# Performance work log

Measured on AMD Instinct MI355X. Metric: run time of the kernel, lower is better.

## Reference

```python
import jax, jax.numpy as jnp
import numpy as np

N = 32768       # nodes
IN = 256        # in_channels
D = 128         # out_channels (per-head dim)
H = 4           # num_heads
M = 4           # num_reps (seeds per partition)
KP = 128        # number of partitions
S = N // KP     # partition size (equal-size partitions)
SCALE = float(np.sqrt(D))


def _linear_init(key, fan_in, fan_out):
    # torch nn.Linear default: U(-1/sqrt(fan_in), 1/sqrt(fan_in)) for W and b
    kw, kb = jax.random.split(key)
    bound = 1.0 / np.sqrt(fan_in)
    w = jax.random.uniform(kw, (fan_in, fan_out), jnp.float32, -bound, bound)
    b = jax.random.uniform(kb, (fan_out,), jnp.float32, -bound, bound)
    return w, b


def setup_inputs() -> dict:
    key = jax.random.key(0)
    k0, k1, k2, k3, k4 = jax.random.split(key, 5)
    x = jax.random.normal(k0, (N, IN), jnp.float32)
    # equal-size disjoint partitions: [KP, S] index array covering 0..N-1
    partition_indices = jnp.arange(N, dtype=jnp.int32).reshape(KP, S)
    Wq_w, Wq_b = _linear_init(k1, IN, H * D)
    Wk_w, Wk_b = _linear_init(k2, IN, H * D)
    Wv_w, Wv_b = _linear_init(k3, IN, H * D)
    pool_seeds = jax.random.normal(k4, (M, H, D), jnp.float32) * 0.02
    alpha_logit = jnp.float32(0.0)
    beta = jnp.float32(1.0)
    return {
        "x": x, "partition_indices": partition_indices,
        "Wq_w": Wq_w, "Wq_b": Wq_b, "Wk_w": Wk_w, "Wk_b": Wk_b,
        "Wv_w": Wv_w, "Wv_b": Wv_b, "pool_seeds": pool_seeds,
        "alpha_logit": alpha_logit, "beta": beta,
    }


def reference(x, partition_indices, Wq_w, Wq_b, Wk_w, Wk_b, Wv_w, Wv_b,
              pool_seeds, alpha_logit, beta):
    n = x.shape[0]
    Q = (x @ Wq_w + Wq_b).reshape(n, H, D)
    K = (x @ Wk_w + Wk_b).reshape(n, H, D)
    V = (x @ Wv_w + Wv_b).reshape(n, H, D)

    # gather per partition -> [KP, S, H, D]
    Qp = Q[partition_indices]
    Kp = K[partition_indices]
    Vp = V[partition_indices]

    # Fine: exact softmax attention within each partition
    attn_local = jnp.einsum('kphd,kqhd->khpq', Qp, Kp) / SCALE
    attn_local = jax.nn.softmax(attn_local, axis=-1)
    outp = jnp.einsum('khpq,kqhd->kphd', attn_local, Vp)  # [KP,S,H,D]
    # partitions are disjoint -> scatter-set back to node order
    out_local = jnp.zeros((n, H, D), x.dtype).at[partition_indices.reshape(-1)].set(
        outp.reshape(n, H, D))
    x_local = out_local.mean(axis=1)  # [N, D]

    # Coarse: learned seeds pool each partition
    pool_attn = jnp.einsum('mhd,kqhd->kmhq', pool_seeds, Kp) / SCALE
    pool_attn = jax.nn.softmax(pool_attn, axis=-1)
    reps_k = jnp.einsum('kmhq,kqhd->kmhd', pool_attn, Kp).reshape(KP * M, H, D)
    reps_v = jnp.einsum('kmhq,kqhd->kmhd', pool_attn, Vp).reshape(KP * M, H, D)

    # Global cross-attention: every node attends to all partition reps
    cross_attn = jnp.einsum('nhd,rhd->nhr', Q, reps_k) / SCALE
    cross_attn = jax.nn.softmax(cross_attn, axis=-1)
    out_global = jnp.einsum('nhr,rhd->nhd', cross_attn, reps_v)
    x_global = out_global.mean(axis=1)  # [N, D]

    x_self = V.mean(axis=1)
    alpha = jax.nn.sigmoid(alpha_logit)
    return alpha * x_local + (1.0 - alpha) * x_global + beta * x_self
```

## Files before the change

kernel.cpp:

```cpp
#include <hip/hip_runtime.h>
#include <hip/hip_bf16.h>


#define INV_SCALE 0.08838834764831845f
#define C2EXP 0.12751744f
#define DEFER_THR 90.50966799f

typedef __attribute__((ext_vector_type(8))) short bf16x8;
typedef __attribute__((ext_vector_type(4))) float floatx4;
typedef unsigned short ushort_t;
typedef unsigned int uint32;

#define OFF_Q    0ull
#define OFF_K    33554432ull
#define OFF_V    67108864ull
#define OFF_LOC  100663296ull
#define OFF_RPK  109051904ull
#define OFF_XC   110100480ull
#define OFF_WC   126877696ull
#define OFF_SCAL 127671296ull
#define OFF_FLAG 127671304ull
#define OFF_RVT  127672320ull
#define OFF_GLB  128196608ull

#define WC_WQ 0
#define WC_WK 131072
#define WC_WV 262144
#define WC_BQ 393216
#define WC_BK 393728
#define WC_BV 394240
#define WC_SEED 394752
#define WC_TOT 396800

static __device__ __forceinline__ float bflo(uint32 u) {
  return __uint_as_float(u << 16);
}
static __device__ __forceinline__ float bfhi(uint32 u) {
  return __uint_as_float(u & 0xffff0000u);
}
static __device__ __forceinline__ float bf2f(ushort_t u) {
  return __uint_as_float(((uint32)u) << 16);
}
static __device__ __forceinline__ ushort_t f2bf(float f) {
  uint32 x = __float_as_uint(f);
  uint32 r = x + 0x7fffu + ((x >> 16) & 1u);
  return (ushort_t)(r >> 16);
}
static __device__ __forceinline__ uint32 pack2bf(float a, float b) {
  return (uint32)f2bf(a) | ((uint32)f2bf(b) << 16);
}
static __device__ __forceinline__ uint32 cvtpk(float a, float b) {
  uint32 r;
  asm("v_cvt_pk_bf16_f32 %0, %1, %2" : "=v"(r) : "v"(a), "v"(b));
  return r;
}

static __device__ __forceinline__ void gl2lds16(const ushort_t* g, ushort_t* l) {
  __builtin_amdgcn_global_load_lds(
      (const __attribute__((address_space(1))) void*)g,
      (__attribute__((address_space(3))) void*)l, 16, 0, 0);
}

__global__ __launch_bounds__(64) void k_detect(const uint32* __restrict__ xw,
                                               const ushort_t* __restrict__ betaRaw,
                                               uint32* __restrict__ flags) {
  const int lane = threadIdx.x;
  const uint32 w = xw[lane * 137 + 3];
  const int e = (w >> 7) & 0xff;
  const unsigned long long b = __ballot(e >= 100 && e <= 140);
  if (lane == 0) {
    flags[0] = (__popcll(b) >= 48) ? 1u : 0u;
    flags[1] = (betaRaw[0] != 0) ? 1u : 0u;
  }
}

static __device__ __forceinline__ void conv8(const void* src, long j, int isB,
                                             ushort_t* dst) {
  if (isB) {
    *reinterpret_cast<uint4*>(dst) =
        *reinterpret_cast<const uint4*>(reinterpret_cast<const ushort_t*>(src) + j);
  } else {
    const float* f = reinterpret_cast<const float*>(src) + j;
    const float4 a = *reinterpret_cast<const float4*>(f);
    const float4 b = *reinterpret_cast<const float4*>(f + 4);
    uint4 o;
    o.x = pack2bf(a.x, a.y); o.y = pack2bf(a.z, a.w);
    o.z = pack2bf(b.x, b.y); o.w = pack2bf(b.z, b.w);
    *reinterpret_cast<uint4*>(dst) = o;
  }
}

__global__ __launch_bounds__(256) void k_convert(
    const void* __restrict__ x,
    const void* __restrict__ Wq, const void* __restrict__ bq,
    const void* __restrict__ Wk, const void* __restrict__ bk,
    const void* __restrict__ Wv, const void* __restrict__ bv,
    const void* __restrict__ seeds, const void* __restrict__ alpha,
    const void* __restrict__ beta,
    ushort_t* __restrict__ xc, ushort_t* __restrict__ wc,
    float* __restrict__ scal, const uint32* __restrict__ flags)
{
  const int isB = (int)flags[0];
  const long i8 = ((long)blockIdx.x * 256 + threadIdx.x) * 8;
  if (blockIdx.y == 0) {
    conv8(x, i8, isB, xc + i8);
  } else {
    if (i8 < WC_BQ) {
      const int sel = (int)(i8 >> 17);
      const long local = i8 & 131071;
      const int kk = (int)(local >> 9);
      const int nn = (int)(local & 511);
      const void* src = sel == 0 ? Wq : (sel == 1 ? Wk : Wv);
      ushort_t* dstW = wc + sel * 131072;
#pragma unroll
      for (int j = 0; j < 8; ++j) {
        ushort_t v;
        if (isB) v = reinterpret_cast<const ushort_t*>(src)[local + j];
        else     v = f2bf(reinterpret_cast<const float*>(src)[local + j]);
        dstW[(size_t)(nn + j) * 256 + kk] = v;
      }
    } else if (i8 < WC_TOT) {
      const void* src; long j;
      if (i8 < WC_BK)        { src = bq;    j = i8 - WC_BQ; }
      else if (i8 < WC_BV)   { src = bk;    j = i8 - WC_BK; }
      else if (i8 < WC_SEED) { src = bv;    j = i8 - WC_BV; }
      else                   { src = seeds; j = i8 - WC_SEED; }
      conv8(src, j, isB, wc + i8);
    }
    if (blockIdx.x == 0 && threadIdx.x == 0) {
      const int isBS = (int)flags[1];
      scal[0] = isBS ? bf2f(reinterpret_cast<const ushort_t*>(alpha)[0])
                     : reinterpret_cast<const float*>(alpha)[0];
      scal[1] = isBS ? bf2f(reinterpret_cast<const ushort_t*>(beta)[0])
                     : reinterpret_cast<const float*>(beta)[0];
    }
  }
}

__global__ __launch_bounds__(256) void k_qkv(
    const ushort_t* __restrict__ xc, const ushort_t* __restrict__ wc,
    ushort_t* __restrict__ Qb, ushort_t* __restrict__ Kb, ushort_t* __restrict__ Vb)
{
  const int m0 = blockIdx.x * 64;
  const int tid = threadIdx.x, lane = tid & 63, wv = tid >> 6;
  const int l16 = lane & 15, quad = lane >> 4;

  __shared__ __align__(16) ushort_t Xs[64 * 256];
  __shared__ __align__(16) ushort_t Ws[64 * 256];

#pragma unroll
  for (int i = 0; i < 8; ++i) {
    const int id = tid + 256 * i;
    const int row = id >> 5, c = id & 31;
    uint4 v = *reinterpret_cast<const uint4*>(xc + (size_t)(m0 + row) * 256 + c * 8);
    *reinterpret_cast<uint4*>(&Xs[row * 256 + ((c ^ (row & 7)) << 3)]) = v;
  }

  for (int sel = 0; sel < 3; ++sel) {
    const ushort_t* WT   = wc + sel * 131072;
    const ushort_t* bias = wc + WC_BQ + sel * 512;
    ushort_t* out        = sel == 0 ? Qb : (sel == 1 ? Kb : Vb);
    for (int nc = 0; nc < 8; ++nc) {
      const int n0 = nc * 64;
      __syncthreads();
#pragma unroll
      for (int i = 0; i < 8; ++i) {
        const int id = tid + 256 * i;
        const int row = id >> 5, c = id & 31;
        uint4 v = *reinterpret_cast<const uint4*>(WT + (size_t)(n0 + row) * 256 + c * 8);
        *reinterpret_cast<uint4*>(&Ws[row * 256 + ((c ^ (row & 7)) << 3)]) = v;
      }
      __syncthreads();

      floatx4 acc[4] = {};
      const int arow = wv * 16 + l16;
#pragma unroll
      for (int ks = 0; ks < 8; ++ks) {
        const int ac = ks * 4 + quad;
        bf16x8 a = *reinterpret_cast<const bf16x8*>(&Xs[arow * 256 + ((ac ^ (arow & 7)) << 3)]);
#pragma unroll
        for (int nt = 0; nt < 4; ++nt) {
          const int brow = nt * 16 + l16;
          bf16x8 b = *reinterpret_cast<const bf16x8*>(&Ws[brow * 256 + ((ac ^ (brow & 7)) << 3)]);
          acc[nt] = __builtin_amdgcn_mfma_f32_16x16x32_bf16(a, b, acc[nt], 0, 0, 0);
        }
      }

#pragma unroll
      for (int nt = 0; nt < 4; ++nt) {
        const int col = n0 + nt * 16 + l16;
        const float bf = bf2f(bias[col]);
#pragma unroll
        for (int r = 0; r < 4; ++r) {
          const int row = m0 + wv * 16 + quad * 4 + r;
          out[(size_t)row * 512 + col] = f2bf(acc[nt][r] + bf);
        }
      }
    }
  }
}

__global__ __launch_bounds__(256) void k_pool(
    const ushort_t* __restrict__ Kb, const ushort_t* __restrict__ Vb,
    const int* __restrict__ pidx_all, const ushort_t* __restrict__ wc,
    ushort_t* __restrict__ rpk, ushort_t* __restrict__ rvT)
{
  const int k = blockIdx.x, h = blockIdx.y;
  const int tid = threadIdx.x, lane = tid & 63, wv = tid >> 6;
  const int* pidx = pidx_all + k * 256;

  __shared__ __align__(16) ushort_t SB[128 * 256];
  const uint32* SBU = reinterpret_cast<const uint32*>(SB);

#pragma unroll
  for (int i = 0; i < 16; ++i) {
    const int e8 = tid + 256 * i;
    const int q = e8 >> 4, dc = (e8 & 15) * 8;
    uint4 kv = *reinterpret_cast<const uint4*>(Kb + (size_t)pidx[q] * 512 + h * 128 + dc);
    const ushort_t* ku = reinterpret_cast<const ushort_t*>(&kv);
    const int qp = q >> 1, qb = q & 1;
#pragma unroll
    for (int j = 0; j < 8; ++j) {
      const int d = dc + j;
      SB[d * 256 + (((qp ^ (d & 31)) << 1) | qb)] = ku[j];
    }
  }
  __syncthreads();

  float q00, q01, q10, q11;
  {
    const uint32* ssrc = reinterpret_cast<const uint32*>(wc + WC_SEED + (size_t)(wv * 4 + h) * 128);
    float s00 = 0.f, s01 = 0.f, s10 = 0.f, s11 = 0.f;
#pragma unroll 8
    for (int dc = 0; dc < 64; ++dc) {
      const uint32 qv = ssrc[dc];
      const float a0 = bflo(qv), a1 = bfhi(qv);
      const int d0 = dc * 2, d1 = d0 + 1;
      const int c0 = lane ^ (d0 & 31);
      const int c1 = lane ^ (d1 & 31);
      const uint32 u00 = SBU[d0 * 128 + c0];
      const uint32 u01 = SBU[d0 * 128 + c0 + 64];
      const uint32 u10 = SBU[d1 * 128 + c1];
      const uint32 u11 = SBU[d1 * 128 + c1 + 64];
      s00 += a0 * bflo(u00) + a1 * bflo(u10);
      s01 += a0 * bfhi(u00) + a1 * bfhi(u10);
      s10 += a0 * bflo(u01) + a1 * bflo(u11);
      s11 += a0 * bfhi(u01) + a1 * bfhi(u11);
    }
    s00 *= INV_SCALE; s01 *= INV_SCALE; s10 *= INV_SCALE; s11 *= INV_SCALE;
    float mx = fmaxf(fmaxf(s00, s01), fmaxf(s10, s11));
#pragma unroll
    for (int off = 32; off >= 1; off >>= 1) mx = fmaxf(mx, __shfl_xor(mx, off));
    const float e00 = __expf(s00 - mx), e01 = __expf(s01 - mx);
    const float e10 = __expf(s10 - mx), e11 = __expf(s11 - mx);
    float sm = e00 + e01 + e10 + e11;
#pragma unroll
    for (int off = 32; off >= 1; off >>= 1) sm += __shfl_xor(sm, off);
    const float inv = 1.0f / sm;
    q00 = e00 * inv; q01 = e01 * inv; q10 = e10 * inv; q11 = e11 * inv;
  }

  {
    float rk0 = 0.f, rk1 = 0.f;
    const int d0 = 2 * lane, d1 = 2 * lane + 1;
#pragma unroll 4
    for (int qp = 0; qp < 64; ++qp) {
      const float pa = __shfl(q00, qp), pb = __shfl(q01, qp);
      const float pc = __shfl(q10, qp), pd = __shfl(q11, qp);
      const int c0 = qp ^ (d0 & 31);
      const int c1 = qp ^ (d1 & 31);
      const uint32 u0  = SBU[d0 * 128 + c0];
      const uint32 u0b = SBU[d0 * 128 + c0 + 64];
      const uint32 u1  = SBU[d1 * 128 + c1];
      const uint32 u1b = SBU[d1 * 128 + c1 + 64];
      rk0 += pa * bflo(u0) + pb * bfhi(u0) + pc * bflo(u0b) + pd * bfhi(u0b);
      rk1 += pa * bflo(u1) + pb * bfhi(u1) + pc * bflo(u1b) + pd * bfhi(u1b);
    }
    reinterpret_cast<uint32*>(rpk + ((size_t)((k * 4 + wv) * 4 + h)) * 128)[lane] = pack2bf(rk0, rk1);
  }
  __syncthreads();

#pragma unroll
  for (int i = 0; i < 16; ++i) {
    const int e8 = tid + 256 * i;
    const int q = e8 >> 4, dc = (e8 & 15) * 8;
    uint4 vv = *reinterpret_cast<const uint4*>(Vb + (size_t)pidx[q] * 512 + h * 128 + dc);
    *reinterpret_cast<uint4*>(&SB[q * 128 + dc]) = vv;
  }
  __syncthreads();

  {
    float rv0 = 0.f, rv1 = 0.f;
#pragma unroll 4
    for (int qp = 0; qp < 64; ++qp) {
      const float pa = __shfl(q00, qp), pb = __shfl(q01, qp);
      const float pc = __shfl(q10, qp), pd = __shfl(q11, qp);
      const uint32 v00 = SBU[(2 * qp) * 64 + lane];
      const uint32 v01 = SBU[(2 * qp + 1) * 64 + lane];
      const uint32 v10 = SBU[(128 + 2 * qp) * 64 + lane];
      const uint32 v11 = SBU[(129 + 2 * qp) * 64 + lane];
      rv0 += pa * bflo(v00) + pb * bflo(v01) + pc * bflo(v10) + pd * bflo(v11);
      rv1 += pa * bfhi(v00) + pb * bfhi(v01) + pc * bfhi(v10) + pd * bfhi(v11);
    }
    const int rrep = k * 4 + wv;
    rvT[(size_t)(h * 128 + 2 * lane) * 512 + rrep]     = f2bf(rv0);
    rvT[(size_t)(h * 128 + 2 * lane + 1) * 512 + rrep] = f2bf(rv1);
  }
}

__global__ __launch_bounds__(256) void k_fine(
    const ushort_t* __restrict__ Qb, const ushort_t* __restrict__ Kb,
    const ushort_t* __restrict__ Vb, const int* __restrict__ pidx_all,
    ushort_t* __restrict__ locS)
{
  const int k = blockIdx.x, qg = blockIdx.y;
  const int tid = threadIdx.x, lane = tid & 63, wv = tid >> 6;
  const int l16 = lane & 15, quad = lane >> 4;
  const int* pidx = pidx_all + k * 256;

  __shared__ __align__(16) ushort_t BsK[2][64 * 128];
  __shared__ __align__(16) ushort_t SBV[128 * 64];
  __shared__ __align__(16) ushort_t Ps[4][16 * 72];

  const int qidx = pidx[qg * 64 + wv * 16 + l16];

  const int kRL = lane >> 4;
  const int kCH = lane & 15;
  const int kswz = l16 & 7;

  float accS[8][4];
#pragma unroll
  for (int nt = 0; nt < 8; ++nt)
#pragma unroll
    for (int r = 0; r < 4; ++r) accS[nt][r] = 0.f;

#pragma unroll
  for (int j = 0; j < 4; ++j) {
    const int row = wv * 16 + j * 4 + kRL;
    gl2lds16(Kb + (size_t)pidx[row] * 512 + ((kCH ^ (row & 7)) << 3),
             &BsK[0][(wv * 16 + j * 4) * 128]);
  }
  __syncthreads();

  bf16x8 qf[4];
  floatx4 O[8];
  float m_i = -3e38f, l_i = 0.f;

  for (int idx = 0; idx < 16; ++idx) {
    const int h = idx >> 2, c = idx & 3;
    const int cur = idx & 1;

    if (c == 0) {
      const ushort_t* qrow = Qb + (size_t)qidx * 512 + h * 128 + quad * 8;
#pragma unroll
      for (int ks = 0; ks < 4; ++ks)
        qf[ks] = *reinterpret_cast<const bf16x8*>(qrow + ks * 32);
#pragma unroll
      for (int nt = 0; nt < 8; ++nt) O[nt] = (floatx4){0.f, 0.f, 0.f, 0.f};
      m_i = -3e38f;
      l_i = 0.f;
    }

    if (idx < 15) {
      const int hn = (idx + 1) >> 2, cn = (idx + 1) & 3;
      const int nb = cur ^ 1;
#pragma unroll
      for (int j = 0; j < 4; ++j) {
        const int row = wv * 16 + j * 4 + kRL;
        gl2lds16(Kb + (size_t)pidx[cn * 64 + row] * 512 + hn * 128 +
                     ((kCH ^ (row & 7)) << 3),
                 &BsK[nb][(wv * 16 + j * 4) * 128]);
      }
    }

    floatx4 S[4] = {};
#pragma unroll
    for (int ks = 0; ks < 4; ++ks) {
      const int ac = ks * 4 + quad;
#pragma unroll
      for (int nt = 0; nt < 4; ++nt) {
        bf16x8 b = *reinterpret_cast<const bf16x8*>(
            &BsK[cur][(nt * 16 + l16) * 128 + ((ac ^ kswz) << 3)]);
        S[nt] = __builtin_amdgcn_mfma_f32_16x16x32_bf16(b, qf[ks], S[nt], 0, 0, 0);
      }
    }

    float cm;
    {
      const float m0 = fmaxf(fmaxf(S[0][0], S[0][1]), fmaxf(S[0][2], S[0][3]));
      const float m1 = fmaxf(fmaxf(S[1][0], S[1][1]), fmaxf(S[1][2], S[1][3]));
      const float m2 = fmaxf(fmaxf(S[2][0], S[2][1]), fmaxf(S[2][2], S[2][3]));
      const float m3 = fmaxf(fmaxf(S[3][0], S[3][1]), fmaxf(S[3][2], S[3][3]));
      cm = fmaxf(fmaxf(m0, m1), fmaxf(m2, m3));
      cm = fmaxf(cm, __shfl_xor(cm, 16));
      cm = fmaxf(cm, __shfl_xor(cm, 32));
    }
    if (!__all(cm <= m_i + DEFER_THR)) {
      const float mn = fmaxf(m_i, cm);
      const float sc = exp2f((m_i - mn) * C2EXP);
      m_i = mn;
      l_i *= sc;
      float scR[4];
#pragma unroll
      for (int r = 0; r < 4; ++r) scR[r] = __shfl(sc, quad * 4 + r);
#pragma unroll
      for (int nt = 0; nt < 8; ++nt)
#pragma unroll
        for (int r = 0; r < 4; ++r) O[nt][r] *= scR[r];
    }
    {
      const float mC = m_i * C2EXP;
      float ps = 0.f;
#pragma unroll
      for (int nt = 0; nt < 4; ++nt) {
        const float p0 = exp2f(S[nt][0] * C2EXP - mC);
        const float p1 = exp2f(S[nt][1] * C2EXP - mC);
        const float p2 = exp2f(S[nt][2] * C2EXP - mC);
        const float p3 = exp2f(S[nt][3] * C2EXP - mC);
        ps += (p0 + p1) + (p2 + p3);
        uint2 pk2 = make_uint2(pack2bf(p0, p1), pack2bf(p2, p3));
        *reinterpret_cast<uint2*>(&Ps[wv][l16 * 72 + nt * 16 + quad * 4]) = pk2;
      }
      ps += __shfl_xor(ps, 16);
      ps += __shfl_xor(ps, 32);
      l_i += ps;
    }

    __syncthreads();
#pragma unroll
    for (int i = 0; i < 4; ++i) {
      const int e = tid + 256 * i;
      const int key = e & 63, dc8 = (e >> 6) * 8;
      uint4 vv = *reinterpret_cast<const uint4*>(
          Vb + (size_t)pidx[c * 64 + key] * 512 + h * 128 + dc8);
      const ushort_t* u = reinterpret_cast<const ushort_t*>(&vv);
#pragma unroll
      for (int j = 0; j < 8; ++j) {
        const int d = dc8 + j;
        SBV[d * 64 + (((key >> 3) ^ j) << 3) + (key & 7)] = u[j];
      }
    }
    __syncthreads();

#pragma unroll
    for (int ks = 0; ks < 2; ++ks) {
      bf16x8 a = *reinterpret_cast<const bf16x8*>(&Ps[wv][l16 * 72 + ks * 32 + quad * 8]);
#pragma unroll
      for (int nt = 0; nt < 8; ++nt) {
        const int d = nt * 16 + l16;
        const int q8 = ks * 4 + quad;
        bf16x8 b = *reinterpret_cast<const bf16x8*>(
            &SBV[d * 64 + ((q8 ^ (d & 7)) << 3)]);
        O[nt] = __builtin_amdgcn_mfma_f32_16x16x32_bf16(a, b, O[nt], 0, 0, 0);
      }
    }

    if (c == 3) {
      float invR[4];
#pragma unroll
      for (int r = 0; r < 4; ++r) invR[r] = 1.0f / __shfl(l_i, quad * 4 + r);
#pragma unroll
      for (int nt = 0; nt < 8; ++nt)
#pragma unroll
        for (int r = 0; r < 4; ++r) accS[nt][r] += O[nt][r] * invR[r];
    }

    __syncthreads();
  }

#pragma unroll
  for (int r = 0; r < 4; ++r) {
    const int n = pidx[qg * 64 + wv * 16 + quad * 4 + r];
#pragma unroll
    for (int nt = 0; nt < 8; ++nt)
      locS[(size_t)n * 128 + nt * 16 + l16] = f2bf(accS[nt][r] * 0.25f);
  }
}

__global__ __launch_bounds__(256, 2) void k_cross(
    const ushort_t* __restrict__ Qb, const ushort_t* __restrict__ rpk,
    const ushort_t* __restrict__ rvT, ushort_t* __restrict__ glb)
{
  const int h = blockIdx.y;
  const int n0 = blockIdx.x * 128;
  const int tid = threadIdx.x, lane = tid & 63, wv = tid >> 6;
  const int l16 = lane & 15, quad = lane >> 4;

  __shared__ __align__(16) ushort_t BsK[2][64 * 128];
  __shared__ __align__(16) ushort_t BsV[2][128 * 64];
  __shared__ __align__(16) ushort_t Ps[4][16 * 72];

  bf16x8 qf0[4], qf1[4];
  {
    const ushort_t* q0 =
        Qb + (size_t)(n0 + wv * 16 + l16) * 512 + h * 128 + quad * 8;
    const ushort_t* q1 = q0 + (size_t)64 * 512;
#pragma unroll
    for (int ks = 0; ks < 4; ++ks) {
      qf0[ks] = *reinterpret_cast<const bf16x8*>(q0 + ks * 32);
      qf1[ks] = *reinterpret_cast<const bf16x8*>(q1 + ks * 32);
    }
  }

  const int kRL = lane >> 4;
  const int kCH = lane & 15;
  const int vDL = lane >> 3;
  const int vCH = lane & 7;

  floatx4 O0[8] = {}, O1[8] = {};
  float m0_i = -3e38f, l0_i = 0.f;
  float m1_i = -3e38f, l1_i = 0.f;

  {
#pragma unroll
    for (int j = 0; j < 4; ++j) {
      const int row = wv * 16 + j * 4 + kRL;
      gl2lds16(rpk + (size_t)row * 512 + h * 128 + ((kCH ^ (row & 7)) << 3),
               &BsK[0][(wv * 16 + j * 4) * 128]);
      const int d = wv * 32 + j * 8 + vDL;
      gl2lds16(rvT + (size_t)(h * 128 + d) * 512 + ((vCH ^ (d & 7)) << 3),
               &BsV[0][(wv * 32 + j * 8) * 64]);
    }
  }
  __syncthreads();

  const int kswz = l16 & 7;

  for (int c = 0; c < 8; ++c) {
    const int cur = c & 1;

    if (c < 7) {
      const int nb = cur ^ 1;
      const int cn = c + 1;
#pragma unroll
      for (int j = 0; j < 4; ++j) {
        const int row = wv * 16 + j * 4 + kRL;
        gl2lds16(rpk + (size_t)(cn * 64 + row) * 512 + h * 128 +
                     ((kCH ^ (row & 7)) << 3),
                 &BsK[nb][(wv * 16 + j * 4) * 128]);
        const int d = wv * 32 + j * 8 + vDL;
        gl2lds16(rvT + (size_t)(h * 128 + d) * 512 + cn * 64 +
                     ((vCH ^ (d & 7)) << 3),
                 &BsV[nb][(wv * 32 + j * 8) * 64]);
      }
    }

#pragma unroll
    for (int s = 0; s < 2; ++s) {
      const bf16x8* qf = (s == 0) ? qf0 : qf1;
      floatx4* O      = (s == 0) ? O0 : O1;
      float& m_i      = (s == 0) ? m0_i : m1_i;
      float& l_i      = (s == 0) ? l0_i : l1_i;

      floatx4 S[4] = {};
#pragma unroll
      for (int ks = 0; ks < 4; ++ks) {
        const int ac = ks * 4 + quad;
#pragma unroll
        for (int nt = 0; nt < 4; ++nt) {
          bf16x8 b = *reinterpret_cast<const bf16x8*>(
              &BsK[cur][(nt * 16 + l16) * 128 + ((ac ^ kswz) << 3)]);
          S[nt] = __builtin_amdgcn_mfma_f32_16x16x32_bf16(b, qf[ks], S[nt], 0, 0, 0);
        }
      }

      float cm;
      {
        const float a0 = fmaxf(fmaxf(S[0][0], S[0][1]), fmaxf(S[0][2], S[0][3]));
        const float a1 = fmaxf(fmaxf(S[1][0], S[1][1]), fmaxf(S[1][2], S[1][3]));
        const float a2 = fmaxf(fmaxf(S[2][0], S[2][1]), fmaxf(S[2][2], S[2][3]));
        const float a3 = fmaxf(fmaxf(S[3][0], S[3][1]), fmaxf(S[3][2], S[3][3]));
        cm = fmaxf(fmaxf(a0, a1), fmaxf(a2, a3));
        cm = fmaxf(cm, __shfl_xor(cm, 16));
        cm = fmaxf(cm, __shfl_xor(cm, 32));
      }
      if (!__all(cm <= m_i + DEFER_THR)) {
        const float mn = fmaxf(m_i, cm);
        const float sc = exp2f((m_i - mn) * C2EXP);
        m_i = mn;
        l_i *= sc;
        float scR[4];
#pragma unroll
        for (int r = 0; r < 4; ++r) scR[r] = __shfl(sc, quad * 4 + r);
#pragma unroll
        for (int nt = 0; nt < 8; ++nt)
#pragma unroll
          for (int r = 0; r < 4; ++r) O[nt][r] *= scR[r];
      }
      {
        const float mC = m_i * C2EXP;
        float ps = 0.f;
#pragma unroll
        for (int nt = 0; nt < 4; ++nt) {
          const float p0 = exp2f(S[nt][0] * C2EXP - mC);
          const float p1 = exp2f(S[nt][1] * C2EXP - mC);
          const float p2 = exp2f(S[nt][2] * C2EXP - mC);
          const float p3 = exp2f(S[nt][3] * C2EXP - mC);
          ps += (p0 + p1) + (p2 + p3);
          uint2 pk2 = make_uint2(cvtpk(p0, p1), cvtpk(p2, p3));
          *reinterpret_cast<uint2*>(&Ps[wv][l16 * 72 + nt * 16 + quad * 4]) = pk2;
        }
        ps += __shfl_xor(ps, 16);
        ps += __shfl_xor(ps, 32);
        l_i += ps;
      }

#pragma unroll
      for (int ks = 0; ks < 2; ++ks) {
        bf16x8 a = *reinterpret_cast<const bf16x8*>(&Ps[wv][l16 * 72 + ks * 32 + quad * 8]);
#pragma unroll
        for (int nt = 0; nt < 8; ++nt) {
          const int q8 = ks * 4 + quad;
          bf16x8 b = *reinterpret_cast<const bf16x8*>(
              &BsV[cur][(nt * 16 + l16) * 64 + ((q8 ^ kswz) << 3)]);
          O[nt] = __builtin_amdgcn_mfma_f32_16x16x32_bf16(a, b, O[nt], 0, 0, 0);
        }
      }
    }

    __syncthreads();
  }

#pragma unroll
  for (int s = 0; s < 2; ++s) {
    const floatx4* O = (s == 0) ? O0 : O1;
    const float l_i  = (s == 0) ? l0_i : l1_i;
    float invR[4];
#pragma unroll
    for (int r = 0; r < 4; ++r) invR[r] = 1.0f / __shfl(l_i, quad * 4 + r);
#pragma unroll
    for (int r = 0; r < 4; ++r) {
      const int n = n0 + s * 64 + wv * 16 + quad * 4 + r;
#pragma unroll
      for (int nt = 0; nt < 8; ++nt)
        glb[(size_t)n * 512 + h * 128 + nt * 16 + l16] = f2bf(O[nt][r] * invR[r]);
    }
  }
}

__global__ __launch_bounds__(256) void k_combine(
    const ushort_t* __restrict__ locS, const ushort_t* __restrict__ glb,
    const ushort_t* __restrict__ Vb, const float* __restrict__ scal,
    float* __restrict__ out)
{
  const int t = blockIdx.x * 256 + threadIdx.x;
  const int n = t >> 6, dp = t & 63;
  const float alpha = 1.0f / (1.0f + __expf(-scal[0]));
  const float beta = scal[1];
  const uint32 lv = reinterpret_cast<const uint32*>(locS)[(size_t)n * 64 + dp];
  float g0 = 0.f, g1 = 0.f, v0 = 0.f, v1 = 0.f;
#pragma unroll
  for (int hh = 0; hh < 4; ++hh) {
    const uint32 gv = *reinterpret_cast<const uint32*>(glb + (size_t)n * 512 + hh * 128 + 2 * dp);
    const uint32 vv = *reinterpret_cast<const uint32*>(Vb + (size_t)n * 512 + hh * 128 + 2 * dp);
    g0 += bflo(gv); g1 += bfhi(gv);
    v0 += bflo(vv); v1 += bfhi(vv);
  }
  const float r0 = alpha * bflo(lv) + (1.0f - alpha) * g0 * 0.25f + beta * v0 * 0.25f;
  const float r1 = alpha * bfhi(lv) + (1.0f - alpha) * g1 * 0.25f + beta * v1 * 0.25f;
  reinterpret_cast<float2*>(out)[(size_t)n * 64 + dp] = make_float2(r0, r1);
}

extern "C" void kernel_launch(void* const* d_in, const int* in_sizes, int n_in,
                              void* d_out, int out_size, void* d_ws, size_t ws_size,
                              hipStream_t stream) {
  const void* x     = d_in[0];
  const int*  pidx  = (const int*)d_in[1];
  const void* Wq    = d_in[2];
  const void* bq    = d_in[3];
  const void* Wk    = d_in[4];
  const void* bk    = d_in[5];
  const void* Wv    = d_in[6];
  const void* bv    = d_in[7];
  const void* seeds = d_in[8];
  const void* al    = d_in[9];
  const void* be    = d_in[10];

  char* ws = (char*)d_ws;
  ushort_t* Qb   = (ushort_t*)(ws + OFF_Q);
  ushort_t* Kb   = (ushort_t*)(ws + OFF_K);
  ushort_t* Vb   = (ushort_t*)(ws + OFF_V);
  ushort_t* locS = (ushort_t*)(ws + OFF_LOC);
  ushort_t* rpk  = (ushort_t*)(ws + OFF_RPK);
  ushort_t* xc   = (ushort_t*)(ws + OFF_XC);
  ushort_t* wc   = (ushort_t*)(ws + OFF_WC);
  float*    scal = (float*)   (ws + OFF_SCAL);
  uint32*   flags= (uint32*)  (ws + OFF_FLAG);
  ushort_t* rvT  = (ushort_t*)(ws + OFF_RVT);
  ushort_t* glb  = (ushort_t*)(ws + OFF_GLB);

  k_detect<<<1, 64, 0, stream>>>((const uint32*)x, (const ushort_t*)be, flags);
  k_convert<<<dim3(4096, 2), 256, 0, stream>>>(x, Wq, bq, Wk, bk, Wv, bv, seeds, al, be,
                                               xc, wc, scal, flags);
  k_qkv<<<512, 256, 0, stream>>>(xc, wc, Qb, Kb, Vb);
  k_pool<<<dim3(128, 4), 256, 0, stream>>>(Kb, Vb, pidx, wc, rpk, rvT);
  k_fine<<<dim3(128, 4), 256, 0, stream>>>(Qb, Kb, Vb, pidx, locS);
  k_cross<<<dim3(256, 4), 256, 0, stream>>>(Qb, rpk, rvT, glb);
  k_combine<<<8192, 256, 0, stream>>>(locS, glb, Vb, scal, (float*)d_out);
}
```

Before: 320.2 us.

## Share K/V LDS fragments across both query halves and single-buffer V tile

Restructures the k_cross loop so each K fragment read from LDS feeds MFMAs for both 64-row query halves, and likewise each V fragment feeds both output accumulators, halving LDS fragment reads. The V tile drops to a single buffer loaded after the PV step, while P gets one buffer per half. The V load for the next chunk is no longer overlapped with compute, and an extra barrier per chunk is added, so V load latency may be exposed, though LDS use falls, which could help occupancy.

Result: no change. 315.5 us (-1.5%).

```diff
diff --git a/kernel.cpp b/kernel.cpp
--- a/kernel.cpp
+++ b/kernel.cpp
@@ -487,8 +487,8 @@
   const int l16 = lane & 15, quad = lane >> 4;
 
   __shared__ __align__(16) ushort_t BsK[2][64 * 128];
-  __shared__ __align__(16) ushort_t BsV[2][128 * 64];
-  __shared__ __align__(16) ushort_t Ps[4][16 * 72];
+  __shared__ __align__(16) ushort_t BsV[128 * 64];
+  __shared__ __align__(16) ushort_t Ps[2][4][16 * 72];
 
   bf16x8 qf0[4], qf1[4];
   {
@@ -519,7 +519,7 @@
                &BsK[0][(wv * 16 + j * 4) * 128]);
       const int d = wv * 32 + j * 8 + vDL;
       gl2lds16(rvT + (size_t)(h * 128 + d) * 512 + ((vCH ^ (d & 7)) << 3),
-               &BsV[0][(wv * 32 + j * 8) * 64]);
+               &BsV[(wv * 32 + j * 8) * 64]);
     }
   }
   __syncthreads();
@@ -538,31 +538,28 @@
         gl2lds16(rpk + (size_t)(cn * 64 + row) * 512 + h * 128 +
                      ((kCH ^ (row & 7)) << 3),
                  &BsK[nb][(wv * 16 + j * 4) * 128]);
-        const int d = wv * 32 + j * 8 + vDL;
-        gl2lds16(rvT + (size_t)(h * 128 + d) * 512 + cn * 64 +
-                     ((vCH ^ (d & 7)) << 3),
-                 &BsV[nb][(wv * 32 + j * 8) * 64]);
+      }
+    }
+
+    floatx4 S0[4] = {}, S1[4] = {};
+#pragma unroll
+    for (int ks = 0; ks < 4; ++ks) {
+      const int ac = ks * 4 + quad;
+#pragma unroll
+      for (int nt = 0; nt < 4; ++nt) {
+        bf16x8 b = *reinterpret_cast<const bf16x8*>(
+            &BsK[cur][(nt * 16 + l16) * 128 + ((ac ^ kswz) << 3)]);
+        S0[nt] = __builtin_amdgcn_mfma_f32_16x16x32_bf16(b, qf0[ks], S0[nt], 0, 0, 0);
+        S1[nt] = __builtin_amdgcn_mfma_f32_16x16x32_bf16(b, qf1[ks], S1[nt], 0, 0, 0);
       }
     }
 
 #pragma unroll
     for (int s = 0; s < 2; ++s) {
-      const bf16x8* qf = (s == 0) ? qf0 : qf1;
+      floatx4* S      = (s == 0) ? S0 : S1;
       floatx4* O      = (s == 0) ? O0 : O1;
       float& m_i      = (s == 0) ? m0_i : m1_i;
       float& l_i      = (s == 0) ? l0_i : l1_i;
-
-      floatx4 S[4] = {};
-#pragma unroll
-      for (int ks = 0; ks < 4; ++ks) {
-        const int ac = ks * 4 + quad;
-#pragma unroll
-        for (int nt = 0; nt < 4; ++nt) {
-          bf16x8 b = *reinterpret_cast<const bf16x8*>(
-              &BsK[cur][(nt * 16 + l16) * 128 + ((ac ^ kswz) << 3)]);
-          S[nt] = __builtin_amdgcn_mfma_f32_16x16x32_bf16(b, qf[ks], S[nt], 0, 0, 0);
-        }
-      }
 
       float cm;
       {
@@ -598,27 +595,42 @@
           const float p3 = exp2f(S[nt][3] * C2EXP - mC);
           ps += (p0 + p1) + (p2 + p3);
           uint2 pk2 = make_uint2(cvtpk(p0, p1), cvtpk(p2, p3));
-          *reinterpret_cast<uint2*>(&Ps[wv][l16 * 72 + nt * 16 + quad * 4]) = pk2;
+          *reinterpret_cast<uint2*>(&Ps[s][wv][l16 * 72 + nt * 16 + quad * 4]) = pk2;
         }
         ps += __shfl_xor(ps, 16);
         ps += __shfl_xor(ps, 32);
         l_i += ps;
       }
-
-#pragma unroll
-      for (int ks = 0; ks < 2; ++ks) {
-        bf16x8 a = *reinterpret_cast<const bf16x8*>(&Ps[wv][l16 * 72 + ks * 32 + quad * 8]);
-#pragma unroll
-        for (int nt = 0; nt < 8; ++nt) {
-          const int q8 = ks * 4 + quad;
-          bf16x8 b = *reinterpret_cast<const bf16x8*>(
-              &BsV[cur][(nt * 16 + l16) * 64 + ((q8 ^ kswz) << 3)]);
-          O[nt] = __builtin_amdgcn_mfma_f32_16x16x32_bf16(a, b, O[nt], 0, 0, 0);
-        }
-      }
     }
 
     __syncthreads();
+
+#pragma unroll
+    for (int ks = 0; ks < 2; ++ks) {
+      bf16x8 a0 = *reinterpret_cast<const bf16x8*>(&Ps[0][wv][l16 * 72 + ks * 32 + quad * 8]);
+      bf16x8 a1 = *reinterpret_cast<const bf16x8*>(&Ps[1][wv][l16 * 72 + ks * 32 + quad * 8]);
+#pragma unroll
+      for (int nt = 0; nt < 8; ++nt) {
+        const int q8 = ks * 4 + quad;
+        bf16x8 b = *reinterpret_cast<const bf16x8*>(
+            &BsV[(nt * 16 + l16) * 64 + ((q8 ^ kswz) << 3)]);
+        O0[nt] = __builtin_amdgcn_mfma_f32_16x16x32_bf16(a0, b, O0[nt], 0, 0, 0);
+        O1[nt] = __builtin_amdgcn_mfma_f32_16x16x32_bf16(a1, b, O1[nt], 0, 0, 0);
+      }
+    }
+
+    __syncthreads();
+
+    if (c < 7) {
+      const int cn = c + 1;
+#pragma unroll
+      for (int j = 0; j < 4; ++j) {
+        const int d = wv * 32 + j * 8 + vDL;
+        gl2lds16(rvT + (size_t)(h * 128 + d) * 512 + cn * 64 +
+                     ((vCH ^ (d & 7)) << 3),
+                 &BsV[(wv * 32 + j * 8) * 64]);
+      }
+    }
   }
 
 #pragma unroll
```
